# Performance work log

Measured on AMD Instinct MI355X. Metric: run time of the kernel, lower is better.

The kernel has to match this reference:

```python
import jax, jax.numpy as jnp
import numpy as np

NACT = 4  # len(activation_list): [linear, cos, sin, tan]


def setup_inputs() -> dict:
    key = jax.random.key(0)
    kx, kw = jax.random.split(key)
    size_in, size_out, batch = 256, 1024, 131072
    x = jax.random.normal(kx, (batch, size_in), dtype=jnp.float32)
    # kaiming_uniform_ with a=sqrt(5): bound = sqrt(6/((1+a^2)*fan_in)) = 1/sqrt(fan_in)
    bound = 1.0 / np.sqrt(size_in)
    weight = jax.random.uniform(kw, (size_out, size_in), dtype=jnp.float32,
                                minval=-bound, maxval=bound)
    return {"x": x, "weight": weight}


def reference(x, weight):
    # linear_combo = x @ W^T : [B, size_out]
    y = jnp.matmul(x, weight.T)
    B, O = y.shape
    # Column j gets activation_list[j % NACT]; reshape so last axis = j % NACT.
    y3 = y.reshape(B, O // NACT, NACT)
    out = jnp.stack(
        [y3[..., 0],            # linear
         jnp.cos(y3[..., 1]),   # cos
         jnp.sin(y3[..., 2]),   # sin
         jnp.tan(y3[..., 3])],  # tan
        axis=-1,
    )
    return out.reshape(B, O)
```

## Files before the change

kernel.cpp:

```cpp
#include <hip/hip_runtime.h>
#include <math.h>

#define BATCH 131072
#define KDIM  256
#define ODIM  1024

#define BM 64
#define BN 64
#define BK 32
#define APAD 4

__global__ __launch_bounds__(256) void gemm_act(
    const float* __restrict__ x,
    const float* __restrict__ w,
    float* __restrict__ out)
{
    __shared__ float As[BK][BM + APAD];
    __shared__ float Bs[BK][BN + APAD];

    const int tid  = threadIdx.x;
    const int col0 = blockIdx.x * BN;
    const int row0 = blockIdx.y * BM;
    const int ty   = tid >> 4;
    const int tx   = tid & 15;

    float acc[4][4] = {};

    for (int k0 = 0; k0 < KDIM; k0 += BK) {
        #pragma unroll
        for (int l = 0; l < 2; ++l) {
            const int f  = tid + l * 256;
            const int r  = f >> 3;
            const int k4 = (f & 7) << 2;
            float4 va = *(const float4*)(x + (size_t)(row0 + r) * KDIM + k0 + k4);
            float4 vb = *(const float4*)(w + (size_t)(col0 + r) * KDIM + k0 + k4);
            As[k4 + 0][r] = va.x; As[k4 + 1][r] = va.y;
            As[k4 + 2][r] = va.z; As[k4 + 3][r] = va.w;
            Bs[k4 + 0][r] = vb.x; Bs[k4 + 1][r] = vb.y;
            Bs[k4 + 2][r] = vb.z; Bs[k4 + 3][r] = vb.w;
        }
        __syncthreads();

        #pragma unroll
        for (int k = 0; k < BK; ++k) {
            float4 a = *(const float4*)&As[k][ty << 2];
            float4 b = *(const float4*)&Bs[k][tx << 2];
            const float ar[4] = {a.x, a.y, a.z, a.w};
            const float br[4] = {b.x, b.y, b.z, b.w};
            #pragma unroll
            for (int i = 0; i < 4; ++i)
                #pragma unroll
                for (int j = 0; j < 4; ++j)
                    acc[i][j] = fmaf(ar[i], br[j], acc[i][j]);
        }
        __syncthreads();
    }

    const int colb = col0 + (tx << 2);
    #pragma unroll
    for (int i = 0; i < 4; ++i) {
        const int row = row0 + (ty << 2) + i;
        const float y0 = acc[i][0];
        const float y1 = acc[i][1];
        const float y2 = acc[i][2];
        const float y3 = acc[i][3];

        float4 o;
        o.x = y0;
        o.y = __cosf(y1);
        o.z = __sinf(y2);
        o.w = tanf(y3);

        const float m    = rintf(y3 * 0.31830988618379067f);
        const float r_   = fmaf(-m, 3.14159265358979323f, y3);
        const float dist = fabsf(fabsf(r_) - 1.57079632679489662f);
        if (dist < 1e-2f) {
            o.w = (float)tan((double)y3);
        }

        *(float4*)(out + (size_t)row * ODIM + colb) = o;
    }
}

extern "C" void kernel_launch(void* const* d_in, const int* in_sizes, int n_in,
                              void* d_out, int out_size, void* d_ws, size_t ws_size,
                              hipStream_t stream)
{
    const float* x = (const float*)d_in[0];
    const float* w = (const float*)d_in[1];
    float* out = (float*)d_out;

    dim3 grid(ODIM / BN, BATCH / BM);
    gemm_act<<<grid, 256, 0, stream>>>(x, w, out);
}
```

Before: 1.415 ms.

## Enlarge GEMM block tile to 128x128 with 8x8 per-thread register tile

Raises the block tile from 64x64 to 128x128 and gives each thread an 8x8 accumulator split into two strided 4-wide halves, so each shared-memory load feeds more FMAs and global traffic per output falls. Tile loading doubles to four float4 loads per thread per K step, and the activation epilogue is restructured to write two float4s per row. The larger accumulator raises register pressure, which may lower occupancy, and the K loop now uses partial unroll 8.

```diff
diff --git a/kernel.cpp b/kernel.cpp
--- a/kernel.cpp
+++ b/kernel.cpp
@@ -5,30 +5,30 @@
 #define KDIM  256
 #define ODIM  1024
 
-#define BM 64
-#define BN 64
+#define BM 128
+#define BN 128
 #define BK 32
-#define APAD 4
+#define PAD 4
 
 __global__ __launch_bounds__(256) void gemm_act(
     const float* __restrict__ x,
     const float* __restrict__ w,
     float* __restrict__ out)
 {
-    __shared__ float As[BK][BM + APAD];
-    __shared__ float Bs[BK][BN + APAD];
+    __shared__ float As[BK][BM + PAD];
+    __shared__ float Bs[BK][BN + PAD];
 
     const int tid  = threadIdx.x;
     const int col0 = blockIdx.x * BN;
     const int row0 = blockIdx.y * BM;
-    const int ty   = tid >> 4;
-    const int tx   = tid & 15;
+    const int ty   = (tid >> 4) << 2;
+    const int tx   = (tid & 15) << 2;
 
-    float acc[4][4] = {};
+    float acc[8][8] = {};
 
     for (int k0 = 0; k0 < KDIM; k0 += BK) {
         #pragma unroll
-        for (int l = 0; l < 2; ++l) {
+        for (int l = 0; l < 4; ++l) {
             const int f  = tid + l * 256;
             const int r  = f >> 3;
             const int k4 = (f & 7) << 2;
@@ -41,44 +41,49 @@
         }
         __syncthreads();
 
-        #pragma unroll
+        #pragma unroll 8
         for (int k = 0; k < BK; ++k) {
-            float4 a = *(const float4*)&As[k][ty << 2];
-            float4 b = *(const float4*)&Bs[k][tx << 2];
-            const float ar[4] = {a.x, a.y, a.z, a.w};
-            const float br[4] = {b.x, b.y, b.z, b.w};
+            float4 a0 = *(const float4*)&As[k][ty];
+            float4 a1 = *(const float4*)&As[k][64 + ty];
+            float4 b0 = *(const float4*)&Bs[k][tx];
+            float4 b1 = *(const float4*)&Bs[k][64 + tx];
+            const float ar[8] = {a0.x, a0.y, a0.z, a0.w, a1.x, a1.y, a1.z, a1.w};
+            const float br[8] = {b0.x, b0.y, b0.z, b0.w, b1.x, b1.y, b1.z, b1.w};
             #pragma unroll
-            for (int i = 0; i < 4; ++i)
+            for (int i = 0; i < 8; ++i)
                 #pragma unroll
-                for (int j = 0; j < 4; ++j)
+                for (int j = 0; j < 8; ++j)
                     acc[i][j] = fmaf(ar[i], br[j], acc[i][j]);
         }
         __syncthreads();
     }
 
-    const int colb = col0 + (tx << 2);
     #pragma unroll
-    for (int i = 0; i < 4; ++i) {
-        const int row = row0 + (ty << 2) + i;
-        const float y0 = acc[i][0];
-        const float y1 = acc[i][1];
-        const float y2 = acc[i][2];
-        const float y3 = acc[i][3];
+    for (int i = 0; i < 8; ++i) {
+        const int row = row0 + (i < 4 ? ty + i : 64 + ty + (i - 4));
+        #pragma unroll
+        for (int jh = 0; jh < 2; ++jh) {
+            const int colb = col0 + jh * 64 + tx;
+            const float y0 = acc[i][jh * 4 + 0];
+            const float y1 = acc[i][jh * 4 + 1];
+            const float y2 = acc[i][jh * 4 + 2];
+            const float y3 = acc[i][jh * 4 + 3];
 
-        float4 o;
-        o.x = y0;
-        o.y = __cosf(y1);
-        o.z = __sinf(y2);
-        o.w = tanf(y3);
+            float4 o;
+            o.x = y0;
+            o.y = __cosf(y1);
+            o.z = __sinf(y2);
+            o.w = tanf(y3);
 
-        const float m    = rintf(y3 * 0.31830988618379067f);
-        const float r_   = fmaf(-m, 3.14159265358979323f, y3);
-        const float dist = fabsf(fabsf(r_) - 1.57079632679489662f);
-        if (dist < 1e-2f) {
-            o.w = (float)tan((double)y3);
+            const float m    = rintf(y3 * 0.31830988618379067f);
+            const float r_   = fmaf(-m, 3.14159265358979323f, y3);
+            const float dist = fabsf(fabsf(r_) - 1.57079632679489662f);
+            if (dist < 1e-2f) {
+                o.w = (float)tan((double)y3);
+            }
+
+            *(float4*)(out + (size_t)row * ODIM + colb) = o;
         }
-
-        *(float4*)(out + (size_t)row * ODIM + colb) = o;
     }
 }
 
```

After: 1.262 ms. 10.8% less time.
